# Performance work log

Measured on AMD Instinct MI355X. Metric: run time of the kernel, lower is better.

Reference implementation:

```python
import jax, jax.numpy as jnp
from jax import lax
import numpy as np


def setup_inputs() -> dict:
    key = jax.random.key(0)
    k1, k2, k3 = jax.random.split(key, 3)
    N, Cin, Cout, H, W, K = 32, 256, 256, 56, 56, 3
    x = jax.random.normal(k1, (N, Cin, H, W), dtype=jnp.float32)
    # xavier_normal-ish init for M (OIHW)
    fan_in, fan_out = Cin * K * K, Cout * K * K
    std = float(np.sqrt(2.0 / (fan_in + fan_out)))
    M = jax.random.normal(k2, (Cout, Cin, K, K), dtype=jnp.float32) * std
    alpha = jax.random.uniform(k3, (Cout, 1, 1), dtype=jnp.float32)
    return {"x": x, "M": M, "alpha": alpha}


def reference(x, M, alpha):
    # Note: the torch module normalizes m.data = m/|m| = sign(m) in-place under
    # no_grad, then applies sign again; sign(sign(M)) == sign(M), so forward is
    # simply a sign-binarized conv scaled by alpha.
    bw = jnp.sign(M)          # binarized weights, OIHW
    ba = jnp.sign(x)          # binarized activations, NCHW
    out = lax.conv_general_dilated(
        ba, bw,
        window_strides=(1, 1),
        padding=[(1, 1), (1, 1)],
        dimension_numbers=("NCHW", "OIHW", "NCHW"),
    )
    return out * alpha  # alpha: (Cout,1,1) broadcasts over (N,Cout,H,W)
```

## Files before the change

### kernel.cpp

```cpp
#include <hip/hip_runtime.h>
#include <stdint.h>


#define CIN  256
#define COUT 256
#define HH   56
#define WW   56
#define NN   32
#define HP   58
#define HWI  (HH*WW)
#define CO_CHUNK 32

typedef unsigned long long u64;
typedef unsigned int u32;

#define XB_BYTES ((size_t)NN*HP*HP*4*8)
#define WB_BYTES ((size_t)COUT*9*4*8)
#define WC_BYTES ((size_t)COUT*9*4)

__global__ __launch_bounds__(256) void pack_w_kernel(const float* __restrict__ M,
                                                     u64* __restrict__ wb,
                                                     u32* __restrict__ wcorr) {
    int co   = blockIdx.x;
    int lane = threadIdx.x & 63;
    int cg   = threadIdx.x >> 6;
    __shared__ u32 pp[9 * 4];
    __shared__ u32 wp[9];

    int c = cg * 64 + lane;
    const float* Mb = M + ((size_t)co * CIN + c) * 9;
    #pragma unroll
    for (int t = 0; t < 9; ++t) {
        float v = Mb[t];
        u64 b = __ballot(v >= 0.0f);
        if (lane == 0) {
            wb[((size_t)co * 9 + t) * 4 + cg] = b;
            pp[t * 4 + cg] = (u32)__popcll(b);
        }
    }
    __syncthreads();
    if (threadIdx.x < 9) {
        int t = threadIdx.x;
        wp[t] = pp[t*4+0] + pp[t*4+1] + pp[t*4+2] + pp[t*4+3];
    }
    __syncthreads();
    if (threadIdx.x < 9) {
        int pid = threadIdx.x;
        int hs = pid / 3, ws = pid % 3;
        u32 corr = 0;
        #pragma unroll
        for (int t = 0; t < 9; ++t) {
            int dh = t / 3 - 1, dw = t % 3 - 1;
            bool inval = (hs == 0 && dh == -1) || (hs == 2 && dh == 1) ||
                         (ws == 0 && dw == -1) || (ws == 2 && dw == 1);
            if (inval) corr += wp[t];
        }
        wcorr[co * 9 + pid] = corr;
    }
}

__global__ __launch_bounds__(256) void pack_x_kernel(const float* __restrict__ x,
                                                     u64* __restrict__ xb) {
    int nh   = blockIdx.x;
    int n    = nh / HH;
    int h    = nh - n * HH;
    int lane = threadIdx.x & 63;
    int cg   = threadIdx.x >> 6;
    int wl   = lane < WW ? lane : WW - 1;

    const float* xr = x + (((size_t)n * CIN + cg * 64) * HH + h) * WW + wl;
    u32 lo = 0, hi = 0;
    #pragma unroll 8
    for (int c = 0; c < 32; ++c) {
        u64 b = __ballot(xr[(size_t)c * HWI] >= 0.0f);
        lo |= (u32)((b >> lane) & 1ull) << c;
    }
    #pragma unroll 8
    for (int c = 0; c < 32; ++c) {
        u64 b = __ballot(xr[(size_t)(c + 32) * HWI] >= 0.0f);
        hi |= (u32)((b >> lane) & 1ull) << c;
    }
    if (lane < WW) {
        u64 acc = ((u64)hi << 32) | lo;
        xb[(((size_t)n * HP + (h + 1)) * HP + (lane + 1)) * 4 + cg] = acc;
    }
}

__global__ __launch_bounds__(256, 2) void conv_kernel(const u64* __restrict__ xb,
                                                      const u64* __restrict__ wb,
                                                      const u32* __restrict__ wcorr,
                                                      const float* __restrict__ alpha,
                                                      float* __restrict__ out) {
    int p   = blockIdx.x * 256 + threadIdx.x;
    int c0  = blockIdx.y * CO_CHUNK;
    int n   = p / HWI;
    int rem = p - n * HWI;
    int h   = rem / WW;
    int w   = rem - h * WW;

    const u64* base = xb + (((size_t)n * HP + h) * HP + w) * 4;
    u64 a[36];
    #pragma unroll
    for (int t = 0; t < 9; ++t) {
        #pragma unroll
        for (int j = 0; j < 4; ++j)
            a[t * 4 + j] = base[((t / 3) * HP + (t % 3)) * 4 + j];
    }
    #pragma unroll
    for (int k = 0; k < 36; ++k) asm volatile("" : "+v"(a[k]));

    int hs = (h == 0) ? 0 : ((h == HH - 1) ? 2 : 1);
    int ws = (w == 0) ? 0 : ((w == WW - 1) ? 2 : 1);
    int pid = hs * 3 + ws;
    int nv  = ((hs == 1) ? 3 : 2) * ((ws == 1) ? 3 : 2);
    int basesum = 256 * nv;

    const u32* wcp = wcorr + pid + (size_t)c0 * 9;
    const float* alp = alpha + c0;
    float* op = out + (size_t)n * COUT * HWI + (size_t)c0 * HWI + rem;

    #pragma unroll 2
    for (int co = 0; co < CO_CHUNK; ++co) {
        const u64* wq = wb + (size_t)(c0 + co) * 36;
        u32 P0 = 0, P1 = 0;
        #pragma unroll
        for (int k = 0; k < 18; ++k) {
            P0 += (u32)__popcll(a[2*k]     ^ wq[2*k]);
            P1 += (u32)__popcll(a[2*k + 1] ^ wq[2*k + 1]);
        }
        u32 P = P0 + P1 - wcp[co * 9];
        float s = (float)(basesum - 2 * (int)P);
        __builtin_nontemporal_store(s * alp[co], &op[(size_t)co * HWI]);
    }
}

extern "C" void kernel_launch(void* const* d_in, const int* in_sizes, int n_in,
                              void* d_out, int out_size, void* d_ws, size_t ws_size,
                              hipStream_t stream) {
    const float* x     = (const float*)d_in[0];
    const float* M     = (const float*)d_in[1];
    const float* alpha = (const float*)d_in[2];
    float* out = (float*)d_out;

    char* ws = (char*)d_ws;
    u64* xb    = (u64*)ws;
    u64* wb    = (u64*)(ws + XB_BYTES);
    u32* wcorr = (u32*)(ws + XB_BYTES + WB_BYTES);

    hipMemsetAsync(xb, 0, XB_BYTES, stream);
    pack_w_kernel<<<COUT, 256, 0, stream>>>(M, wb, wcorr);
    pack_x_kernel<<<NN * HH, 256, 0, stream>>>(x, xb);
    dim3 cgrid((NN * HWI) / 256, COUT / CO_CHUNK);
    conv_kernel<<<cgrid, 256, 0, stream>>>(xb, wb, wcorr, alpha, out);
}
```

Baseline: 300.2 us.

## Stage chunk weights in LDS, use 32-bit popcounts, raise occupancy

The conv kernel now loads the 32-output-channel weight chunk into shared memory once per block, instead of having every thread read it from global memory. Activations are loaded with 128-bit vector loads into 32-bit registers, and 32-bit popcounts feed four accumulators. Launch bounds move to 4 blocks per SM, the correction table is transposed so per-channel reads are contiguous, and the pack_x unroll grows. The risks are more register pressure (72 u32 registers) under the tighter occupancy bound, and LDS broadcast reads taking the place of scalar cached loads.

```diff
diff --git a/kernel.cpp b/kernel.cpp
--- a/kernel.cpp
+++ b/kernel.cpp
@@ -16,7 +16,7 @@
 
 #define XB_BYTES ((size_t)NN*HP*HP*4*8)
 #define WB_BYTES ((size_t)COUT*9*4*8)
-#define WC_BYTES ((size_t)COUT*9*4)
+#define WC_BYTES ((size_t)9*COUT*4)
 
 __global__ __launch_bounds__(256) void pack_w_kernel(const float* __restrict__ M,
                                                      u64* __restrict__ wb,
@@ -55,7 +55,7 @@
                          (ws == 0 && dw == -1) || (ws == 2 && dw == 1);
             if (inval) corr += wp[t];
         }
-        wcorr[co * 9 + pid] = corr;
+        wcorr[pid * COUT + co] = corr;
     }
 }
 
@@ -70,12 +70,12 @@
 
     const float* xr = x + (((size_t)n * CIN + cg * 64) * HH + h) * WW + wl;
     u32 lo = 0, hi = 0;
-    #pragma unroll 8
+    #pragma unroll 16
     for (int c = 0; c < 32; ++c) {
         u64 b = __ballot(xr[(size_t)c * HWI] >= 0.0f);
         lo |= (u32)((b >> lane) & 1ull) << c;
     }
-    #pragma unroll 8
+    #pragma unroll 16
     for (int c = 0; c < 32; ++c) {
         u64 b = __ballot(xr[(size_t)(c + 32) * HWI] >= 0.0f);
         hi |= (u32)((b >> lane) & 1ull) << c;
@@ -86,50 +86,67 @@
     }
 }
 
-__global__ __launch_bounds__(256, 2) void conv_kernel(const u64* __restrict__ xb,
+__global__ __launch_bounds__(256, 4) void conv_kernel(const u64* __restrict__ xb,
                                                       const u64* __restrict__ wb,
                                                       const u32* __restrict__ wcorr,
                                                       const float* __restrict__ alpha,
                                                       float* __restrict__ out) {
-    int p   = blockIdx.x * 256 + threadIdx.x;
+    __shared__ u32 w_lds[CO_CHUNK * 72];
+
+    int tid = threadIdx.x;
+    int p   = blockIdx.x * 256 + tid;
     int c0  = blockIdx.y * CO_CHUNK;
     int n   = p / HWI;
     int rem = p - n * HWI;
     int h   = rem / WW;
     int w   = rem - h * WW;
 
-    const u64* base = xb + (((size_t)n * HP + h) * HP + w) * 4;
-    u64 a[36];
+    const uint4* wsrc = (const uint4*)(wb + (size_t)c0 * 36);
+    uint4* wdst = (uint4*)w_lds;
+    uint4 s0 = wsrc[tid];
+    uint4 s1 = wsrc[tid + 256];
+    uint4 s2 = wsrc[512 + (tid & 63)];
+
+    const u32* base = (const u32*)(xb + (((size_t)n * HP + h) * HP + w) * 4);
+    u32 a[72];
     #pragma unroll
     for (int t = 0; t < 9; ++t) {
-        #pragma unroll
-        for (int j = 0; j < 4; ++j)
-            a[t * 4 + j] = base[((t / 3) * HP + (t % 3)) * 4 + j];
+        const uint4* tb = (const uint4*)(base + ((t / 3) * HP + (t % 3)) * 8);
+        uint4 v0 = tb[0], v1 = tb[1];
+        a[t*8+0]=v0.x; a[t*8+1]=v0.y; a[t*8+2]=v0.z; a[t*8+3]=v0.w;
+        a[t*8+4]=v1.x; a[t*8+5]=v1.y; a[t*8+6]=v1.z; a[t*8+7]=v1.w;
     }
+
+    wdst[tid]       = s0;
+    wdst[tid + 256] = s1;
+    if (tid < 64) wdst[512 + tid] = s2;
+    __syncthreads();
+
     #pragma unroll
-    for (int k = 0; k < 36; ++k) asm volatile("" : "+v"(a[k]));
+    for (int k = 0; k < 72; ++k) asm volatile("" : "+v"(a[k]));
 
     int hs = (h == 0) ? 0 : ((h == HH - 1) ? 2 : 1);
     int ws = (w == 0) ? 0 : ((w == WW - 1) ? 2 : 1);
     int pid = hs * 3 + ws;
     int nv  = ((hs == 1) ? 3 : 2) * ((ws == 1) ? 3 : 2);
-    int basesum = 256 * nv;
+    float basesum = (float)(256 * nv);
 
-    const u32* wcp = wcorr + pid + (size_t)c0 * 9;
+    const u32* wcp = wcorr + pid * COUT + c0;
     const float* alp = alpha + c0;
     float* op = out + (size_t)n * COUT * HWI + (size_t)c0 * HWI + rem;
 
-    #pragma unroll 2
     for (int co = 0; co < CO_CHUNK; ++co) {
-        const u64* wq = wb + (size_t)(c0 + co) * 36;
-        u32 P0 = 0, P1 = 0;
+        const u32* wq = &w_lds[co * 72];
+        u32 P0 = 0, P1 = 0, P2 = 0, P3 = 0;
         #pragma unroll
-        for (int k = 0; k < 18; ++k) {
-            P0 += (u32)__popcll(a[2*k]     ^ wq[2*k]);
-            P1 += (u32)__popcll(a[2*k + 1] ^ wq[2*k + 1]);
+        for (int k = 0; k < 72; k += 4) {
+            P0 += __builtin_popcount(a[k]     ^ wq[k]);
+            P1 += __builtin_popcount(a[k + 1] ^ wq[k + 1]);
+            P2 += __builtin_popcount(a[k + 2] ^ wq[k + 2]);
+            P3 += __builtin_popcount(a[k + 3] ^ wq[k + 3]);
         }
-        u32 P = P0 + P1 - wcp[co * 9];
-        float s = (float)(basesum - 2 * (int)P);
+        u32 P = (P0 + P1) + (P2 + P3) - wcp[co];
+        float s = basesum - 2.0f * (float)(int)P;
         __builtin_nontemporal_store(s * alp[co], &op[(size_t)co * HWI]);
     }
 }
```

Result: faster. 293.1 us (-2.3%).
